# Kernel tuning notes

Hardware: AMD Instinct MI355X
Metric: run time of the kernel (lower is better)

The kernel has to match this reference:

```python
import jax, jax.numpy as jnp
import numpy as np

CL = 64      # per-object feature dim
N = 8        # num objects/slots
B = 8192     # batch


def _init(key, fan_in, shape):
    # torch Linear default: U(-1/sqrt(fan_in), 1/sqrt(fan_in))
    bound = 1.0 / np.sqrt(fan_in)
    return jax.random.uniform(key, shape, jnp.float32, -bound, bound)


def setup_inputs() -> dict:
    key = jax.random.key(0)
    ks = jax.random.split(key, 20)
    inp = {
        "s": jax.random.normal(ks[0], (B, N, CL), jnp.float32),
        # weights stored (in, out); y = x @ W + b
        "W_enc": _init(ks[1], CL, (CL, CL)),   "b_enc": _init(ks[2], CL, (CL,)),
        "W_self0": _init(ks[3], CL, (CL, CL)), "b_self0": _init(ks[4], CL, (CL,)),
        "W_self1": _init(ks[5], CL, (CL, CL)), "b_self1": _init(ks[6], CL, (CL,)),
        "W_rel0": _init(ks[7], 2 * CL + 1, (2 * CL + 1, 2 * CL)), "b_rel0": _init(ks[8], 2 * CL + 1, (2 * CL,)),
        "W_rel1": _init(ks[9], 2 * CL, (2 * CL, CL)),             "b_rel1": _init(ks[10], 2 * CL, (CL,)),
        "W_rel2": _init(ks[11], CL, (CL, CL)),                    "b_rel2": _init(ks[12], CL, (CL,)),
        "W_att0": _init(ks[13], 2 * CL + 1, (2 * CL + 1, 2 * CL)), "b_att0": _init(ks[14], 2 * CL + 1, (2 * CL,)),
        "W_att1": _init(ks[15], 2 * CL, (2 * CL, CL)),             "b_att1": _init(ks[16], 2 * CL, (CL,)),
        "W_att2": _init(ks[17], CL, (CL, 1)),                      "b_att2": _init(ks[18], CL, (1,)),
    }
    return inp


def reference(s, W_enc, b_enc, W_self0, b_self0, W_self1, b_self1,
              W_rel0, b_rel0, W_rel1, b_rel1, W_rel2, b_rel2,
              W_att0, b_att0, W_att1, b_att1, W_att2, b_att2):
    elu = jax.nn.elu
    # keep first 2 coords (positions), re-encode the rest
    s = jnp.concatenate([s[..., :2], (s @ W_enc + b_enc)[..., 2:]], axis=-1)  # [B,N,CL]

    # self dynamics
    h = elu(s @ W_self0 + b_self0)
    self_dyn = h @ W_self1 + b_self1 + h                                      # [B,N,CL]

    # pairwise squared distances on first two coords: [B,N,N,1]
    pos = s[..., :2]
    dist = jnp.sum((pos[:, :, None, :] - pos[:, None, :, :]) ** 2, axis=-1, keepdims=True)

    # combinations = cat(arg1_i, arg2_j, dist). Split the first linear's weight rows
    # so we never materialize the [B,N,N,2CL+1] concat tensor.
    def pair_linear(W, b):
        Wa, Wb, Wd = W[:CL], W[CL:2 * CL], W[2 * CL]
        return (s @ Wa)[:, :, None, :] + (s @ Wb)[:, None, :, :] + dist * Wd + b

    rel_h1 = elu(pair_linear(W_rel0, b_rel0))        # [B,N,N,2CL]
    rel_h2 = elu(rel_h1 @ W_rel1 + b_rel1)           # [B,N,N,CL]
    rel_f = rel_h2 @ W_rel2 + b_rel2 + rel_h2        # [B,N,N,CL]

    att = elu(pair_linear(W_att0, b_att0))
    att = elu(att @ W_att1 + b_att1)
    att = jax.nn.sigmoid(att @ W_att2 + b_att2)      # [B,N,N,1]

    diag_mask = (1.0 - jnp.eye(N, dtype=s.dtype))[None, :, :, None]
    rel_dyn = jnp.sum(rel_f * diag_mask * att, axis=2)   # [B,N,CL]

    return jnp.sum(self_dyn + rel_dyn, axis=1)           # [B,CL]
```

## Files before the change

kernel.cpp:

```cpp
#include <hip/hip_runtime.h>
#include <math.h>

constexpr int NCL = 64;
constexpr int NN  = 8;
constexpr int NG  = 2;
constexpr int NT  = 512;

typedef __attribute__((ext_vector_type(4))) float f32x4;
typedef __attribute__((ext_vector_type(8))) short s16x8;
#define MFMA __builtin_amdgcn_mfma_f32_16x16x32_bf16

constexpr int OFF_ENC = 0;
constexpr int OFF_S0  = 1024;
constexpr int OFF_S1  = 2048;
constexpr int OFF_R0  = 3072;
constexpr int OFF_A0  = 7168;
constexpr int OFF_A1  = 11264;
constexpr int OFF_R1  = 13312;
constexpr int OFF_R2  = 15360;

__device__ __forceinline__ float elu_f(float x) { return x > 0.f ? x : __expf(x) - 1.f; }

__device__ __forceinline__ unsigned f2u(float x) { union { float f; unsigned u; } c; c.f = x; return c.u; }
__device__ __forceinline__ float u2f(unsigned u) { union { unsigned u; float f; } c; c.u = u; return c.f; }

__device__ __forceinline__ void splitpack8(const float v[8], s16x8& hi, s16x8& lo) {
    union { s16x8 s; unsigned u[4]; } H, L;
    #pragma unroll
    for (int e = 0; e < 8; e += 2) {
        H.u[e >> 1] = __builtin_amdgcn_perm(f2u(v[e + 1]), f2u(v[e]), 0x07060302u);
        const float t0 = u2f(f2u(v[e])     & 0xffff0000u);
        const float t1 = u2f(f2u(v[e + 1]) & 0xffff0000u);
        L.u[e >> 1] = __builtin_amdgcn_perm(f2u(v[e + 1] - t1), f2u(v[e] - t0), 0x07060302u);
    }
    hi = H.s; lo = L.s;
}

__device__ __forceinline__ void afrag_split(const float* act, int row, int kbase,
                                            s16x8& hi, s16x8& lo) {
    const float4 v0 = *(const float4*)(act + row * 68 + kbase);
    const float4 v1 = *(const float4*)(act + row * 68 + kbase + 4);
    const float v[8] = {v0.x, v0.y, v0.z, v0.w, v1.x, v1.y, v1.z, v1.w};
    splitpack8(v, hi, lo);
}

__device__ __forceinline__ f32x4 node_tile_pk(const float* act, const s16x8* __restrict__ wb,
                                              int mt, int nt, int lane) {
    const int row = mt * 16 + (lane & 15);
    const int g   = lane >> 4;
    f32x4 acc = {0.f, 0.f, 0.f, 0.f};
    #pragma unroll
    for (int kg = 0; kg < 2; ++kg) {
        s16x8 ah, al;
        afrag_split(act, row, kg * 32 + g * 8, ah, al);
        const s16x8 bh = wb[(kg * 4 + nt) * 64 + lane];
        const s16x8 bl = wb[512 + (kg * 4 + nt) * 64 + lane];
        acc = MFMA(ah, bh, acc, 0, 0, 0);
        acc = MFMA(ah, bl, acc, 0, 0, 0);
        acc = MFMA(al, bh, acc, 0, 0, 0);
    }
    return acc;
}

__device__ __forceinline__ void x1frag(const float* Arow, const float* Brow,
                                       const float* wdg, float d, int fbase,
                                       s16x8& hi, s16x8& lo) {
    const float4 a0 = *(const float4*)(Arow + fbase);
    const float4 a1 = *(const float4*)(Arow + fbase + 4);
    const float4 c0 = *(const float4*)(Brow + fbase);
    const float4 c1 = *(const float4*)(Brow + fbase + 4);
    const float4 w0 = *(const float4*)(wdg + fbase);
    const float4 w1 = *(const float4*)(wdg + fbase + 4);
    float v[8];
    v[0] = elu_f(fmaf(d, w0.x, a0.x + c0.x));
    v[1] = elu_f(fmaf(d, w0.y, a0.y + c0.y));
    v[2] = elu_f(fmaf(d, w0.z, a0.z + c0.z));
    v[3] = elu_f(fmaf(d, w0.w, a0.w + c0.w));
    v[4] = elu_f(fmaf(d, w1.x, a1.x + c1.x));
    v[5] = elu_f(fmaf(d, w1.y, a1.y + c1.y));
    v[6] = elu_f(fmaf(d, w1.z, a1.z + c1.z));
    v[7] = elu_f(fmaf(d, w1.w, a1.w + c1.w));
    splitpack8(v, hi, lo);
}

__device__ __forceinline__ short bfh_rn(float x) {
    union { float f; unsigned u; } c; c.f = x;
    return (short)((c.u + 0x7fffu + ((c.u >> 16) & 1u)) >> 16);
}
__device__ __forceinline__ void split_tr(float x, short& hi, short& lo) {
    union { float f; unsigned u; } c; c.f = x;
    hi = (short)(c.u >> 16);
    union { unsigned u; float f; } t; t.u = c.u & 0xffff0000u;
    lo = bfh_rn(x - t.f);
}

__global__ __launch_bounds__(64)
void prep_kernel(const float* __restrict__ We,  const float* __restrict__ Ws0,
                 const float* __restrict__ Ws1, const float* __restrict__ Wr0,
                 const float* __restrict__ Wa0, const float* __restrict__ Wa1,
                 const float* __restrict__ Wr1, const float* __restrict__ Wr2,
                 s16x8* __restrict__ ws)
{
    const int b = blockIdx.x, lane = threadIdx.x;
    const float* W; int nnt, nfrag, base, frag;
    if      (b < 8)   { W = We;  nnt = 4; nfrag = 8;  base = OFF_ENC; frag = b; }
    else if (b < 16)  { W = Ws0; nnt = 4; nfrag = 8;  base = OFF_S0;  frag = b - 8; }
    else if (b < 24)  { W = Ws1; nnt = 4; nfrag = 8;  base = OFF_S1;  frag = b - 16; }
    else if (b < 56)  { W = Wr0; nnt = 8; nfrag = 32; base = OFF_R0;  frag = b - 24; }
    else if (b < 88)  { W = Wa0; nnt = 8; nfrag = 32; base = OFF_A0;  frag = b - 56; }
    else if (b < 104) { W = Wa1; nnt = 4; nfrag = 16; base = OFF_A1;  frag = b - 88; }
    else if (b < 120) { W = Wr1; nnt = 4; nfrag = 16; base = OFF_R1;  frag = b - 104; }
    else              { W = Wr2; nnt = 4; nfrag = 8;  base = OFF_R2;  frag = b - 120; }
    const int kg = frag / nnt, nt = frag % nnt;
    const int N  = nnt * 16;
    const int g  = lane >> 4, col = nt * 16 + (lane & 15);
    s16x8 hi, lo;
    #pragma unroll
    for (int e = 0; e < 8; ++e) {
        short a, c; split_tr(W[(kg * 32 + g * 8 + e) * N + col], a, c);
        hi[e] = a; lo[e] = c;
    }
    ws[base + frag * 64 + lane]              = hi;
    ws[base + nfrag * 64 + frag * 64 + lane] = lo;
}

__global__ __launch_bounds__(NT, 6)
void gh_kernel(const float* __restrict__ S,
               const float* __restrict__ b_enc,
               const float* __restrict__ b_self0, const float* __restrict__ b_self1,
               const float* __restrict__ W_rel0,  const float* __restrict__ b_rel0,
               const float* __restrict__ b_rel1,  const float* __restrict__ b_rel2,
               const float* __restrict__ W_att0,  const float* __restrict__ b_att0,
               const float* __restrict__ b_att1,
               const float* __restrict__ W_att2,  const float* __restrict__ b_att2,
               const s16x8* __restrict__ wp,
               float* __restrict__ Out)
{
    __shared__ __align__(16) float sbuf[16 * 68];
    __shared__ __align__(16) float encb[16 * 68];
    __shared__ __align__(16) float hbuf[16 * 68];
    __shared__ __align__(16) float ABm[4][16 * 132];
    __shared__ float d2l[2 * 64];
    __shared__ float cntl[16];
    __shared__ float wdl[2][128];

    const int tid  = threadIdx.x;
    const int w    = tid >> 6;
    const int lane = tid & 63;
    const int g    = lane >> 4;
    const int b0   = blockIdx.x * NG;
    float* sd   = sbuf;
    float* Tb   = hbuf;
    float* Ubuf = encb;
    float* Rbuf = encb + 512;

    {
        const float* src = S + (size_t)b0 * NN * NCL;
        for (int idx = tid; idx < 16 * 64; idx += NT)
            sbuf[(idx >> 6) * 68 + (idx & 63)] = src[idx];
        if (tid < 128) {
            wdl[0][tid] = W_rel0[128 * 128 + tid];
            wdl[1][tid] = W_att0[128 * 128 + tid];
        }
    }
    __syncthreads();

    if (tid < 128) {
        const int bi = tid >> 6, i = (tid >> 3) & 7, j = tid & 7;
        const float dx = sbuf[(bi * 8 + i) * 68 + 0] - sbuf[(bi * 8 + j) * 68 + 0];
        const float dy = sbuf[(bi * 8 + i) * 68 + 1] - sbuf[(bi * 8 + j) * 68 + 1];
        d2l[bi * 64 + i * 8 + j] = dx * dx + dy * dy;
    }

    if (w < 4) {
        const int nt = w;
        f32x4 acc = node_tile_pk(sbuf, wp + OFF_ENC, 0, nt, lane);
        const int   col = nt * 16 + (lane & 15);
        const float be  = b_enc[col];
        #pragma unroll
        for (int reg = 0; reg < 4; ++reg) {
            const int row = g * 4 + reg;
            float v = acc[reg] + be;
            if (col < 2) v = sbuf[row * 68 + col];
            encb[row * 68 + col] = v;
        }
    }
    __syncthreads();

    if (w < 4) {
        const int nt = w;
        f32x4 acc = node_tile_pk(encb, wp + OFF_S0, 0, nt, lane);
        const int   col = nt * 16 + (lane & 15);
        const float bs  = b_self0[col];
        #pragma unroll
        for (int reg = 0; reg < 4; ++reg)
            hbuf[(g * 4 + reg) * 68 + col] = elu_f(acc[reg] + bs);
    }
    __syncthreads();

    if (w < 4) {
        const int nt = w;
        f32x4 acc = node_tile_pk(hbuf, wp + OFF_S1, 0, nt, lane);
        const int   col = nt * 16 + (lane & 15);
        const float bs  = b_self1[col];
        #pragma unroll
        for (int reg = 0; reg < 4; ++reg) {
            const int row = g * 4 + reg;
            sd[row * 68 + col] = acc[reg] + bs + hbuf[row * 68 + col];
        }
    }
    {
        const int ntp = w;
        const int row = lane & 15;
        const int col = ntp * 16 + (lane & 15);
        s16x8 eh[2], el[2];
        afrag_split(encb, row, g * 8, eh[0], el[0]);
        afrag_split(encb, row, 32 + g * 8, eh[1], el[1]);
        #pragma unroll
        for (int m = 0; m < 4; ++m) {
            const s16x8* wb = wp + ((m < 2) ? OFF_R0 : OFF_A0);
            const int kgo = (m & 1) * 2;
            f32x4 acc = {0.f, 0.f, 0.f, 0.f};
            #pragma unroll
            for (int kg = 0; kg < 2; ++kg) {
                const s16x8 bh = wb[((kgo + kg) * 8 + ntp) * 64 + lane];
                const s16x8 bl = wb[2048 + ((kgo + kg) * 8 + ntp) * 64 + lane];
                acc = MFMA(eh[kg], bh, acc, 0, 0, 0);
                acc = MFMA(eh[kg], bl, acc, 0, 0, 0);
                acc = MFMA(el[kg], bh, acc, 0, 0, 0);
            }
            const float badd = (m == 0) ? b_rel0[col] : (m == 2) ? b_att0[col] : 0.f;
            #pragma unroll
            for (int reg = 0; reg < 4; ++reg)
                ABm[m][(g * 4 + reg) * 132 + col] = acc[reg] + badd;
        }
    }
    __syncthreads();

    const int bi    = w >> 2;
    const int ihalf = (w >> 1) & 1;
    const int mt    = w & 1;
    const int pp    = (lane & 15) + 16 * mt;
    const int il    = pp >> 3, jj8 = pp & 7;
    const float* Arow_a = &ABm[2][(bi * 8 + ihalf * 4 + il) * 132];
    const float* Brow_a = &ABm[3][(bi * 8 + jj8) * 132];
    const float* Arow_r = &ABm[0][(bi * 8 + ihalf * 4 + il) * 132];
    const float* Brow_r = &ABm[1][(bi * 8 + jj8) * 132];
    const float dpair   = d2l[bi * 64 + (ihalf * 4 + il) * 8 + jj8];

    float attreg[4];
    {
        const float ba2 = b_att2[0];
        float wa2v[4];
        f32x4 acc[4];
        #pragma unroll
        for (int nt = 0; nt < 4; ++nt) {
            wa2v[nt] = W_att2[nt * 16 + (lane & 15)];
            const float b1 = b_att1[nt * 16 + (lane & 15)];
            acc[nt] = {b1, b1, b1, b1};
        }
        #pragma unroll
        for (int kg = 0; kg < 4; ++kg) {
            s16x8 ah, al;
            x1frag(Arow_a, Brow_a, &wdl[1][0], dpair, kg * 32 + g * 8, ah, al);
            #pragma unroll
            for (int nt = 0; nt < 4; ++nt) {
                const s16x8 bh = wp[OFF_A1 + (kg * 4 + nt) * 64 + lane];
                const s16x8 bl = wp[OFF_A1 + 1024 + (kg * 4 + nt) * 64 + lane];
                acc[nt] = MFMA(ah, bh, acc[nt], 0, 0, 0);
                acc[nt] = MFMA(ah, bl, acc[nt], 0, 0, 0);
                acc[nt] = MFMA(al, bh, acc[nt], 0, 0, 0);
            }
        }
        #pragma unroll
        for (int reg = 0; reg < 4; ++reg) {
            float s = 0.f;
            #pragma unroll
            for (int nt = 0; nt < 4; ++nt) s += elu_f(acc[nt][reg]) * wa2v[nt];
            s += __shfl_xor(s, 1, 64);
            s += __shfl_xor(s, 2, 64);
            s += __shfl_xor(s, 4, 64);
            s += __shfl_xor(s, 8, 64);
            attreg[reg] = 1.f / (1.f + __expf(-(s + ba2)));
        }
    }
    {
        f32x4 acc[4];
        #pragma unroll
        for (int nt = 0; nt < 4; ++nt) {
            const float b1 = b_rel1[nt * 16 + (lane & 15)];
            acc[nt] = {b1, b1, b1, b1};
        }
        #pragma unroll
        for (int kg = 0; kg < 4; ++kg) {
            s16x8 ah, al;
            x1frag(Arow_r, Brow_r, &wdl[0][0], dpair, kg * 32 + g * 8, ah, al);
            #pragma unroll
            for (int nt = 0; nt < 4; ++nt) {
                const s16x8 bh = wp[OFF_R1 + (kg * 4 + nt) * 64 + lane];
                const s16x8 bl = wp[OFF_R1 + 1024 + (kg * 4 + nt) * 64 + lane];
                acc[nt] = MFMA(ah, bh, acc[nt], 0, 0, 0);
                acc[nt] = MFMA(ah, bl, acc[nt], 0, 0, 0);
                acc[nt] = MFMA(al, bh, acc[nt], 0, 0, 0);
            }
        }
        const int ifull = ihalf * 4 + 2 * mt + (g >> 1);
        float coef[4], cpart = 0.f;
        #pragma unroll
        for (int reg = 0; reg < 4; ++reg) {
            const int jj = 4 * (g & 1) + reg;
            coef[reg] = (jj == ifull) ? 0.f : attreg[reg];
            cpart += coef[reg];
        }
        const float csum = cpart + __shfl_xor(cpart, 16, 64);
        if (((g & 1) == 0) && ((lane & 15) == 0))
            cntl[bi * 8 + ifull] = csum;
        #pragma unroll
        for (int nt = 0; nt < 4; ++nt) {
            float tpart = 0.f;
            #pragma unroll
            for (int reg = 0; reg < 4; ++reg)
                tpart += coef[reg] * elu_f(acc[nt][reg]);
            const float tsum = tpart + __shfl_xor(tpart, 16, 64);
            if ((g & 1) == 0)
                Tb[(bi * 8 + ifull) * 68 + nt * 16 + (lane & 15)] = tsum;
        }
    }
    __syncthreads();

    if (tid < 128) {
        const int b = tid >> 6, c = tid & 63;
        float u = 0.f;
        #pragma unroll
        for (int i = 0; i < 8; ++i) u += Tb[(b * 8 + i) * 68 + c];
        Ubuf[b * 68 + c] = u;
    }
    __syncthreads();

    if (w < 4) {
        const int nt2 = w;
        f32x4 acc = {0.f, 0.f, 0.f, 0.f};
        const int row = lane & 15;
        #pragma unroll
        for (int kg = 0; kg < 2; ++kg) {
            float4 q0 = {0.f, 0.f, 0.f, 0.f}, q1 = {0.f, 0.f, 0.f, 0.f};
            if (row < 2) {
                q0 = *(const float4*)(Ubuf + row * 68 + kg * 32 + g * 8);
                q1 = *(const float4*)(Ubuf + row * 68 + kg * 32 + g * 8 + 4);
            }
            const float v[8] = {q0.x, q0.y, q0.z, q0.w, q1.x, q1.y, q1.z, q1.w};
            s16x8 uh, ul;
            splitpack8(v, uh, ul);
            const s16x8 bh = wp[OFF_R2 + (kg * 4 + nt2) * 64 + lane];
            const s16x8 bl = wp[OFF_R2 + 512 + (kg * 4 + nt2) * 64 + lane];
            acc = MFMA(uh, bh, acc, 0, 0, 0);
            acc = MFMA(uh, bl, acc, 0, 0, 0);
            acc = MFMA(ul, bh, acc, 0, 0, 0);
        }
        if (g == 0) {
            #pragma unroll
            for (int reg = 0; reg < 2; ++reg)
                Rbuf[reg * 64 + nt2 * 16 + (lane & 15)] = acc[reg];
        }
    }
    __syncthreads();

    if (tid < 128) {
        const int b = tid >> 6, c = tid & 63;
        float sds = 0.f, C = 0.f;
        #pragma unroll
        for (int i = 0; i < 8; ++i) {
            sds += sd[(b * 8 + i) * 68 + c];
            C   += cntl[b * 8 + i];
        }
        Out[(size_t)(b0 + b) * 64 + c] = sds + Rbuf[b * 64 + c] + C * b_rel2[c] + Ubuf[b * 68 + c];
    }
}

extern "C" void kernel_launch(void* const* d_in, const int* in_sizes, int n_in,
                              void* d_out, int out_size, void* d_ws, size_t ws_size,
                              hipStream_t stream) {
    const float* S       = (const float*)d_in[0];
    const float* W_enc   = (const float*)d_in[1];
    const float* b_enc   = (const float*)d_in[2];
    const float* W_self0 = (const float*)d_in[3];
    const float* b_self0 = (const float*)d_in[4];
    const float* W_self1 = (const float*)d_in[5];
    const float* b_self1 = (const float*)d_in[6];
    const float* W_rel0  = (const float*)d_in[7];
    const float* b_rel0  = (const float*)d_in[8];
    const float* W_rel1  = (const float*)d_in[9];
    const float* b_rel1  = (const float*)d_in[10];
    const float* W_rel2  = (const float*)d_in[11];
    const float* b_rel2  = (const float*)d_in[12];
    const float* W_att0  = (const float*)d_in[13];
    const float* b_att0  = (const float*)d_in[14];
    const float* W_att1  = (const float*)d_in[15];
    const float* b_att1  = (const float*)d_in[16];
    const float* W_att2  = (const float*)d_in[17];
    const float* b_att2  = (const float*)d_in[18];

    s16x8* wpk = (s16x8*)d_ws;

    prep_kernel<<<dim3(128), dim3(64), 0, stream>>>(
        W_enc, W_self0, W_self1, W_rel0, W_att0, W_att1, W_rel1, W_rel2, wpk);

    const int nB   = in_sizes[0] / (NN * NCL);
    const int grid = nB / NG;

    gh_kernel<<<dim3(grid), dim3(NT), 0, stream>>>(
        S, b_enc, b_self0, b_self1,
        W_rel0, b_rel0, b_rel1, b_rel2,
        W_att0, b_att0, b_att1, W_att2, b_att2,
        wpk, (float*)d_out);
}
```

Baseline: 209.0 us.

## Halve pairwise LDS buffer by time-sharing att/rel projections, raise occupancy, pack f32x2 math

The shared ABm buffer is cut from four to two slices. The attention-branch projections are computed first and consumed, then the relation-branch projections are recomputed into the same slices after a barrier. This reduces LDS per block so the launch bound can ask for 8 blocks per CU instead of 6. The elementwise split and ELU fragment building now use 2-wide float vectors, which may map to packed FP32 instructions. The cost is an extra barrier phase, recomputing the encoder A-fragments, and tighter register limits that could cause spills.

```diff
diff --git a/kernel.cpp b/kernel.cpp
--- a/kernel.cpp
+++ b/kernel.cpp
@@ -7,6 +7,7 @@
 constexpr int NT  = 512;
 
 typedef __attribute__((ext_vector_type(4))) float f32x4;
+typedef __attribute__((ext_vector_type(2))) float f32x2;
 typedef __attribute__((ext_vector_type(8))) short s16x8;
 #define MFMA __builtin_amdgcn_mfma_f32_16x16x32_bf16
 
@@ -29,9 +30,9 @@
     #pragma unroll
     for (int e = 0; e < 8; e += 2) {
         H.u[e >> 1] = __builtin_amdgcn_perm(f2u(v[e + 1]), f2u(v[e]), 0x07060302u);
-        const float t0 = u2f(f2u(v[e])     & 0xffff0000u);
-        const float t1 = u2f(f2u(v[e + 1]) & 0xffff0000u);
-        L.u[e >> 1] = __builtin_amdgcn_perm(f2u(v[e + 1] - t1), f2u(v[e] - t0), 0x07060302u);
+        f32x2 t = {u2f(f2u(v[e]) & 0xffff0000u), u2f(f2u(v[e + 1]) & 0xffff0000u)};
+        f32x2 r = (f32x2){v[e], v[e + 1]} - t;
+        L.u[e >> 1] = __builtin_amdgcn_perm(f2u(r.y), f2u(r.x), 0x07060302u);
     }
     hi = H.s; lo = L.s;
 }
@@ -71,16 +72,21 @@
     const float4 c1 = *(const float4*)(Brow + fbase + 4);
     const float4 w0 = *(const float4*)(wdg + fbase);
     const float4 w1 = *(const float4*)(wdg + fbase + 4);
-    float v[8];
-    v[0] = elu_f(fmaf(d, w0.x, a0.x + c0.x));
-    v[1] = elu_f(fmaf(d, w0.y, a0.y + c0.y));
-    v[2] = elu_f(fmaf(d, w0.z, a0.z + c0.z));
-    v[3] = elu_f(fmaf(d, w0.w, a0.w + c0.w));
-    v[4] = elu_f(fmaf(d, w1.x, a1.x + c1.x));
-    v[5] = elu_f(fmaf(d, w1.y, a1.y + c1.y));
-    v[6] = elu_f(fmaf(d, w1.z, a1.z + c1.z));
-    v[7] = elu_f(fmaf(d, w1.w, a1.w + c1.w));
-    splitpack8(v, hi, lo);
+    const f32x2 A2[4] = {{a0.x, a0.y}, {a0.z, a0.w}, {a1.x, a1.y}, {a1.z, a1.w}};
+    const f32x2 C2[4] = {{c0.x, c0.y}, {c0.z, c0.w}, {c1.x, c1.y}, {c1.z, c1.w}};
+    const f32x2 W2[4] = {{w0.x, w0.y}, {w0.z, w0.w}, {w1.x, w1.y}, {w1.z, w1.w}};
+    const f32x2 dd = {d, d};
+    union { s16x8 s; unsigned u[4]; } H, L;
+    #pragma unroll
+    for (int p = 0; p < 4; ++p) {
+        const f32x2 t = __builtin_elementwise_fma(dd, W2[p], A2[p] + C2[p]);
+        const float v0 = elu_f(t.x), v1 = elu_f(t.y);
+        H.u[p] = __builtin_amdgcn_perm(f2u(v1), f2u(v0), 0x07060302u);
+        const f32x2 tr = {u2f(f2u(v0) & 0xffff0000u), u2f(f2u(v1) & 0xffff0000u)};
+        const f32x2 r  = (f32x2){v0, v1} - tr;
+        L.u[p] = __builtin_amdgcn_perm(f2u(r.y), f2u(r.x), 0x07060302u);
+    }
+    hi = H.s; lo = L.s;
 }
 
 __device__ __forceinline__ short bfh_rn(float x) {
@@ -124,7 +130,7 @@
     ws[base + nfrag * 64 + frag * 64 + lane] = lo;
 }
 
-__global__ __launch_bounds__(NT, 6)
+__global__ __launch_bounds__(NT, 8)
 void gh_kernel(const float* __restrict__ S,
                const float* __restrict__ b_enc,
                const float* __restrict__ b_self0, const float* __restrict__ b_self1,
@@ -139,7 +145,7 @@
     __shared__ __align__(16) float sbuf[16 * 68];
     __shared__ __align__(16) float encb[16 * 68];
     __shared__ __align__(16) float hbuf[16 * 68];
-    __shared__ __align__(16) float ABm[4][16 * 132];
+    __shared__ __align__(16) float ABm[2][16 * 132];
     __shared__ float d2l[2 * 64];
     __shared__ float cntl[16];
     __shared__ float wdl[2][128];
@@ -217,19 +223,18 @@
         afrag_split(encb, row, g * 8, eh[0], el[0]);
         afrag_split(encb, row, 32 + g * 8, eh[1], el[1]);
         #pragma unroll
-        for (int m = 0; m < 4; ++m) {
-            const s16x8* wb = wp + ((m < 2) ? OFF_R0 : OFF_A0);
-            const int kgo = (m & 1) * 2;
+        for (int m = 0; m < 2; ++m) {
+            const int kgo = m * 2;
             f32x4 acc = {0.f, 0.f, 0.f, 0.f};
             #pragma unroll
             for (int kg = 0; kg < 2; ++kg) {
-                const s16x8 bh = wb[((kgo + kg) * 8 + ntp) * 64 + lane];
-                const s16x8 bl = wb[2048 + ((kgo + kg) * 8 + ntp) * 64 + lane];
+                const s16x8 bh = wp[OFF_A0 + ((kgo + kg) * 8 + ntp) * 64 + lane];
+                const s16x8 bl = wp[OFF_A0 + 2048 + ((kgo + kg) * 8 + ntp) * 64 + lane];
                 acc = MFMA(eh[kg], bh, acc, 0, 0, 0);
                 acc = MFMA(eh[kg], bl, acc, 0, 0, 0);
                 acc = MFMA(el[kg], bh, acc, 0, 0, 0);
             }
-            const float badd = (m == 0) ? b_rel0[col] : (m == 2) ? b_att0[col] : 0.f;
+            const float badd = (m == 0) ? b_att0[col] : 0.f;
             #pragma unroll
             for (int reg = 0; reg < 4; ++reg)
                 ABm[m][(g * 4 + reg) * 132 + col] = acc[reg] + badd;
@@ -242,11 +247,9 @@
     const int mt    = w & 1;
     const int pp    = (lane & 15) + 16 * mt;
     const int il    = pp >> 3, jj8 = pp & 7;
-    const float* Arow_a = &ABm[2][(bi * 8 + ihalf * 4 + il) * 132];
-    const float* Brow_a = &ABm[3][(bi * 8 + jj8) * 132];
-    const float* Arow_r = &ABm[0][(bi * 8 + ihalf * 4 + il) * 132];
-    const float* Brow_r = &ABm[1][(bi * 8 + jj8) * 132];
-    const float dpair   = d2l[bi * 64 + (ihalf * 4 + il) * 8 + jj8];
+    const float* Arow = &ABm[0][(bi * 8 + ihalf * 4 + il) * 132];
+    const float* Brow = &ABm[1][(bi * 8 + jj8) * 132];
+    const float dpair = d2l[bi * 64 + (ihalf * 4 + il) * 8 + jj8];
 
     float attreg[4];
     {
@@ -262,7 +265,7 @@
         #pragma unroll
         for (int kg = 0; kg < 4; ++kg) {
             s16x8 ah, al;
-            x1frag(Arow_a, Brow_a, &wdl[1][0], dpair, kg * 32 + g * 8, ah, al);
+            x1frag(Arow, Brow, &wdl[1][0], dpair, kg * 32 + g * 8, ah, al);
             #pragma unroll
             for (int nt = 0; nt < 4; ++nt) {
                 const s16x8 bh = wp[OFF_A1 + (kg * 4 + nt) * 64 + lane];
@@ -284,6 +287,35 @@
             attreg[reg] = 1.f / (1.f + __expf(-(s + ba2)));
         }
     }
+    __syncthreads();
+
+    {
+        const int ntp = w;
+        const int row = lane & 15;
+        const int col = ntp * 16 + (lane & 15);
+        s16x8 eh[2], el[2];
+        afrag_split(encb, row, g * 8, eh[0], el[0]);
+        afrag_split(encb, row, 32 + g * 8, eh[1], el[1]);
+        #pragma unroll
+        for (int m = 0; m < 2; ++m) {
+            const int kgo = m * 2;
+            f32x4 acc = {0.f, 0.f, 0.f, 0.f};
+            #pragma unroll
+            for (int kg = 0; kg < 2; ++kg) {
+                const s16x8 bh = wp[OFF_R0 + ((kgo + kg) * 8 + ntp) * 64 + lane];
+                const s16x8 bl = wp[OFF_R0 + 2048 + ((kgo + kg) * 8 + ntp) * 64 + lane];
+                acc = MFMA(eh[kg], bh, acc, 0, 0, 0);
+                acc = MFMA(eh[kg], bl, acc, 0, 0, 0);
+                acc = MFMA(el[kg], bh, acc, 0, 0, 0);
+            }
+            const float badd = (m == 0) ? b_rel0[col] : 0.f;
+            #pragma unroll
+            for (int reg = 0; reg < 4; ++reg)
+                ABm[m][(g * 4 + reg) * 132 + col] = acc[reg] + badd;
+        }
+    }
+    __syncthreads();
+
     {
         f32x4 acc[4];
         #pragma unroll
@@ -294,7 +326,7 @@
         #pragma unroll
         for (int kg = 0; kg < 4; ++kg) {
             s16x8 ah, al;
-            x1frag(Arow_r, Brow_r, &wdl[0][0], dpair, kg * 32 + g * 8, ah, al);
+            x1frag(Arow, Brow, &wdl[0][0], dpair, kg * 32 + g * 8, ah, al);
             #pragma unroll
             for (int nt = 0; nt < 4; ++nt) {
                 const s16x8 bh = wp[OFF_R1 + (kg * 4 + nt) * 64 + lane];
```

Result: slower. 240.0 us (+14.8%).

## Split attention and relation pair MLPs across wave groups, share B-row loads

Applied to the files above, without the earlier changes.

Before, every wave computed both the attention and the relation pair MLP for one 16-row tile. Now waves 0-3 compute only attention and waves 4-7 only relation, each handling two M-tiles that share the B-row, distance-weight and weight-fragment loads. Attention coefficients pass between the groups through a new small shared buffer and an extra barrier. Packed float2 (f32x2) arithmetic is also added in the split/elu fragment building, which may let the compiler emit packed FP32 instructions. In exchange, per-wave register pressure goes up from holding two accumulator sets, and the added barrier stalls relation waves until the attention waves finish.

```diff
diff --git a/kernel.cpp b/kernel.cpp
--- a/kernel.cpp
+++ b/kernel.cpp
@@ -7,6 +7,7 @@
 constexpr int NT  = 512;
 
 typedef __attribute__((ext_vector_type(4))) float f32x4;
+typedef __attribute__((ext_vector_type(2))) float f32x2;
 typedef __attribute__((ext_vector_type(8))) short s16x8;
 #define MFMA __builtin_amdgcn_mfma_f32_16x16x32_bf16
 
@@ -29,9 +30,9 @@
     #pragma unroll
     for (int e = 0; e < 8; e += 2) {
         H.u[e >> 1] = __builtin_amdgcn_perm(f2u(v[e + 1]), f2u(v[e]), 0x07060302u);
-        const float t0 = u2f(f2u(v[e])     & 0xffff0000u);
-        const float t1 = u2f(f2u(v[e + 1]) & 0xffff0000u);
-        L.u[e >> 1] = __builtin_amdgcn_perm(f2u(v[e + 1] - t1), f2u(v[e] - t0), 0x07060302u);
+        f32x2 t = {u2f(f2u(v[e]) & 0xffff0000u), u2f(f2u(v[e + 1]) & 0xffff0000u)};
+        f32x2 r = (f32x2){v[e], v[e + 1]} - t;
+        L.u[e >> 1] = __builtin_amdgcn_perm(f2u(r.y), f2u(r.x), 0x07060302u);
     }
     hi = H.s; lo = L.s;
 }
@@ -62,25 +63,27 @@
     return acc;
 }
 
-__device__ __forceinline__ void x1frag(const float* Arow, const float* Brow,
-                                       const float* wdg, float d, int fbase,
-                                       s16x8& hi, s16x8& lo) {
+__device__ __forceinline__ void x1build(const float* Arow, int fbase,
+                                        const float4 b0, const float4 b1,
+                                        const float4 w0, const float4 w1, float d,
+                                        s16x8& hi, s16x8& lo) {
     const float4 a0 = *(const float4*)(Arow + fbase);
     const float4 a1 = *(const float4*)(Arow + fbase + 4);
-    const float4 c0 = *(const float4*)(Brow + fbase);
-    const float4 c1 = *(const float4*)(Brow + fbase + 4);
-    const float4 w0 = *(const float4*)(wdg + fbase);
-    const float4 w1 = *(const float4*)(wdg + fbase + 4);
-    float v[8];
-    v[0] = elu_f(fmaf(d, w0.x, a0.x + c0.x));
-    v[1] = elu_f(fmaf(d, w0.y, a0.y + c0.y));
-    v[2] = elu_f(fmaf(d, w0.z, a0.z + c0.z));
-    v[3] = elu_f(fmaf(d, w0.w, a0.w + c0.w));
-    v[4] = elu_f(fmaf(d, w1.x, a1.x + c1.x));
-    v[5] = elu_f(fmaf(d, w1.y, a1.y + c1.y));
-    v[6] = elu_f(fmaf(d, w1.z, a1.z + c1.z));
-    v[7] = elu_f(fmaf(d, w1.w, a1.w + c1.w));
-    splitpack8(v, hi, lo);
+    const f32x2 A2[4] = {{a0.x, a0.y}, {a0.z, a0.w}, {a1.x, a1.y}, {a1.z, a1.w}};
+    const f32x2 C2[4] = {{b0.x, b0.y}, {b0.z, b0.w}, {b1.x, b1.y}, {b1.z, b1.w}};
+    const f32x2 W2[4] = {{w0.x, w0.y}, {w0.z, w0.w}, {w1.x, w1.y}, {w1.z, w1.w}};
+    const f32x2 dd = {d, d};
+    union { s16x8 s; unsigned u[4]; } H, L;
+    #pragma unroll
+    for (int p = 0; p < 4; ++p) {
+        const f32x2 t = __builtin_elementwise_fma(dd, W2[p], A2[p] + C2[p]);
+        const float v0 = elu_f(t.x), v1 = elu_f(t.y);
+        H.u[p] = __builtin_amdgcn_perm(f2u(v1), f2u(v0), 0x07060302u);
+        const f32x2 tr = {u2f(f2u(v0) & 0xffff0000u), u2f(f2u(v1) & 0xffff0000u)};
+        const f32x2 r  = (f32x2){v0, v1} - tr;
+        L.u[p] = __builtin_amdgcn_perm(f2u(r.y), f2u(r.x), 0x07060302u);
+    }
+    hi = H.s; lo = L.s;
 }
 
 __device__ __forceinline__ short bfh_rn(float x) {
@@ -143,6 +146,7 @@
     __shared__ float d2l[2 * 64];
     __shared__ float cntl[16];
     __shared__ float wdl[2][128];
+    __shared__ __align__(16) float attl[2][8][8];
 
     const int tid  = threadIdx.x;
     const int w    = tid >> 6;
@@ -237,93 +241,104 @@
     }
     __syncthreads();
 
-    const int bi    = w >> 2;
-    const int ihalf = (w >> 1) & 1;
-    const int mt    = w & 1;
-    const int pp    = (lane & 15) + 16 * mt;
-    const int il    = pp >> 3, jj8 = pp & 7;
-    const float* Arow_a = &ABm[2][(bi * 8 + ihalf * 4 + il) * 132];
-    const float* Brow_a = &ABm[3][(bi * 8 + jj8) * 132];
-    const float* Arow_r = &ABm[0][(bi * 8 + ihalf * 4 + il) * 132];
-    const float* Brow_r = &ABm[1][(bi * 8 + jj8) * 132];
-    const float dpair   = d2l[bi * 64 + (ihalf * 4 + il) * 8 + jj8];
-
-    float attreg[4];
+    const int isRel = w >> 2;
+    const int wl    = w & 3;
+    const int bi    = wl >> 1;
+    const int ihalf = wl & 1;
+    const int il0   = (lane & 15) >> 3;
+    const int jj8   = lane & 7;
+    const int mA    = isRel ? 0 : 2;
+    const float* Arow0 = &ABm[mA][(bi * 8 + ihalf * 4 + il0) * 132];
+    const float* Arow1 = Arow0 + 2 * 132;
+    const float* Brow  = &ABm[mA + 1][(bi * 8 + jj8) * 132];
+    const float* wdg   = &wdl[isRel ? 0 : 1][0];
+    const float  d0    = d2l[bi * 64 + (ihalf * 4 + il0) * 8 + jj8];
+    const float  d1    = d2l[bi * 64 + (ihalf * 4 + il0 + 2) * 8 + jj8];
+    const s16x8* wfr   = wp + (isRel ? OFF_R1 : OFF_A1);
+
+    f32x4 acc0[4], acc1[4];
     {
+        const float* bias = isRel ? b_rel1 : b_att1;
+        #pragma unroll
+        for (int nt = 0; nt < 4; ++nt) {
+            const float b1 = bias[nt * 16 + (lane & 15)];
+            acc0[nt] = {b1, b1, b1, b1};
+            acc1[nt] = {b1, b1, b1, b1};
+        }
+        #pragma unroll
+        for (int kg = 0; kg < 4; ++kg) {
+            const int fbase = kg * 32 + g * 8;
+            const float4 c0 = *(const float4*)(Brow + fbase);
+            const float4 c1 = *(const float4*)(Brow + fbase + 4);
+            const float4 w0 = *(const float4*)(wdg + fbase);
+            const float4 w1 = *(const float4*)(wdg + fbase + 4);
+            s16x8 ah0, al0, ah1, al1;
+            x1build(Arow0, fbase, c0, c1, w0, w1, d0, ah0, al0);
+            x1build(Arow1, fbase, c0, c1, w0, w1, d1, ah1, al1);
+            #pragma unroll
+            for (int nt = 0; nt < 4; ++nt) {
+                const s16x8 bh = wfr[(kg * 4 + nt) * 64 + lane];
+                const s16x8 bl = wfr[1024 + (kg * 4 + nt) * 64 + lane];
+                acc0[nt] = MFMA(ah0, bh, acc0[nt], 0, 0, 0);
+                acc0[nt] = MFMA(ah0, bl, acc0[nt], 0, 0, 0);
+                acc0[nt] = MFMA(al0, bh, acc0[nt], 0, 0, 0);
+                acc1[nt] = MFMA(ah1, bh, acc1[nt], 0, 0, 0);
+                acc1[nt] = MFMA(ah1, bl, acc1[nt], 0, 0, 0);
+                acc1[nt] = MFMA(al1, bh, acc1[nt], 0, 0, 0);
+            }
+        }
+    }
+
+    if (!isRel) {
         const float ba2 = b_att2[0];
         float wa2v[4];
-        f32x4 acc[4];
-        #pragma unroll
-        for (int nt = 0; nt < 4; ++nt) {
-            wa2v[nt] = W_att2[nt * 16 + (lane & 15)];
-            const float b1 = b_att1[nt * 16 + (lane & 15)];
-            acc[nt] = {b1, b1, b1, b1};
-        }
-        #pragma unroll
-        for (int kg = 0; kg < 4; ++kg) {
-            s16x8 ah, al;
-            x1frag(Arow_a, Brow_a, &wdl[1][0], dpair, kg * 32 + g * 8, ah, al);
+        #pragma unroll
+        for (int nt = 0; nt < 4; ++nt) wa2v[nt] = W_att2[nt * 16 + (lane & 15)];
+        #pragma unroll
+        for (int mt = 0; mt < 2; ++mt) {
+            const f32x4* acc = mt ? acc1 : acc0;
+            const int i = ihalf * 4 + 2 * mt + (g >> 1);
+            float am[4], cpart = 0.f;
+            #pragma unroll
+            for (int reg = 0; reg < 4; ++reg) {
+                float s = 0.f;
+                #pragma unroll
+                for (int nt = 0; nt < 4; ++nt) s += elu_f(acc[nt][reg]) * wa2v[nt];
+                s += __shfl_xor(s, 1, 64);
+                s += __shfl_xor(s, 2, 64);
+                s += __shfl_xor(s, 4, 64);
+                s += __shfl_xor(s, 8, 64);
+                const float a = 1.f / (1.f + __expf(-(s + ba2)));
+                const int jj  = 4 * (g & 1) + reg;
+                am[reg] = (jj == i) ? 0.f : a;
+                cpart  += am[reg];
+            }
+            const float csum = cpart + __shfl_xor(cpart, 16, 64);
+            if ((lane & 15) == 0) {
+                *(float4*)&attl[bi][i][4 * (g & 1)] = (float4){am[0], am[1], am[2], am[3]};
+                if ((g & 1) == 0) cntl[bi * 8 + i] = csum;
+            }
+        }
+    }
+    __syncthreads();
+
+    if (isRel) {
+        #pragma unroll
+        for (int mt = 0; mt < 2; ++mt) {
+            const f32x4* acc = mt ? acc1 : acc0;
+            const int i = ihalf * 4 + 2 * mt + (g >> 1);
+            const float4 cf = *(const float4*)&attl[bi][i][4 * (g & 1)];
+            const float coef[4] = {cf.x, cf.y, cf.z, cf.w};
             #pragma unroll
             for (int nt = 0; nt < 4; ++nt) {
-                const s16x8 bh = wp[OFF_A1 + (kg * 4 + nt) * 64 + lane];
-                const s16x8 bl = wp[OFF_A1 + 1024 + (kg * 4 + nt) * 64 + lane];
-                acc[nt] = MFMA(ah, bh, acc[nt], 0, 0, 0);
-                acc[nt] = MFMA(ah, bl, acc[nt], 0, 0, 0);
-                acc[nt] = MFMA(al, bh, acc[nt], 0, 0, 0);
-            }
-        }
-        #pragma unroll
-        for (int reg = 0; reg < 4; ++reg) {
-            float s = 0.f;
-            #pragma unroll
-            for (int nt = 0; nt < 4; ++nt) s += elu_f(acc[nt][reg]) * wa2v[nt];
-            s += __shfl_xor(s, 1, 64);
-            s += __shfl_xor(s, 2, 64);
-            s += __shfl_xor(s, 4, 64);
-            s += __shfl_xor(s, 8, 64);
-            attreg[reg] = 1.f / (1.f + __expf(-(s + ba2)));
-        }
-    }
-    {
-        f32x4 acc[4];
-        #pragma unroll
-        for (int nt = 0; nt < 4; ++nt) {
-            const float b1 = b_rel1[nt * 16 + (lane & 15)];
-            acc[nt] = {b1, b1, b1, b1};
-        }
-        #pragma unroll
-        for (int kg = 0; kg < 4; ++kg) {
-            s16x8 ah, al;
-            x1frag(Arow_r, Brow_r, &wdl[0][0], dpair, kg * 32 + g * 8, ah, al);
-            #pragma unroll
-            for (int nt = 0; nt < 4; ++nt) {
-                const s16x8 bh = wp[OFF_R1 + (kg * 4 + nt) * 64 + lane];
-                const s16x8 bl = wp[OFF_R1 + 1024 + (kg * 4 + nt) * 64 + lane];
-                acc[nt] = MFMA(ah, bh, acc[nt], 0, 0, 0);
-                acc[nt] = MFMA(ah, bl, acc[nt], 0, 0, 0);
-                acc[nt] = MFMA(al, bh, acc[nt], 0, 0, 0);
-            }
-        }
-        const int ifull = ihalf * 4 + 2 * mt + (g >> 1);
-        float coef[4], cpart = 0.f;
-        #pragma unroll
-        for (int reg = 0; reg < 4; ++reg) {
-            const int jj = 4 * (g & 1) + reg;
-            coef[reg] = (jj == ifull) ? 0.f : attreg[reg];
-            cpart += coef[reg];
-        }
-        const float csum = cpart + __shfl_xor(cpart, 16, 64);
-        if (((g & 1) == 0) && ((lane & 15) == 0))
-            cntl[bi * 8 + ifull] = csum;
-        #pragma unroll
-        for (int nt = 0; nt < 4; ++nt) {
-            float tpart = 0.f;
-            #pragma unroll
-            for (int reg = 0; reg < 4; ++reg)
-                tpart += coef[reg] * elu_f(acc[nt][reg]);
-            const float tsum = tpart + __shfl_xor(tpart, 16, 64);
-            if ((g & 1) == 0)
-                Tb[(bi * 8 + ifull) * 68 + nt * 16 + (lane & 15)] = tsum;
+                float tpart = 0.f;
+                #pragma unroll
+                for (int reg = 0; reg < 4; ++reg)
+                    tpart += coef[reg] * elu_f(acc[nt][reg]);
+                const float tsum = tpart + __shfl_xor(tpart, 16, 64);
+                if ((g & 1) == 0)
+                    Tb[(bi * 8 + i) * 68 + nt * 16 + (lane & 15)] = tsum;
+            }
         }
     }
     __syncthreads();
```

Result: no change. 211.8 us (+1.4%).
